# Performance work log

Measured on AMD Instinct MI355X. Metric: run time of the kernel, lower is better.

Reference implementation:

```python
import jax, jax.numpy as jnp
import numpy as np


def setup_inputs() -> dict:
    key = jax.random.key(0)
    ks = jax.random.split(key, 8)
    B, L, D, H = 4, 2048, 4096, 8
    BW = D // H
    std = 1.0 / np.sqrt(BW)
    x = jax.random.normal(ks[0], (B, L, D), dtype=jnp.float32)
    segment_pos = jax.random.randint(ks[1], (B, L), 0, 1024)
    prev_h = jax.random.normal(ks[2], (B, D), dtype=jnp.float32)
    w_in = jax.random.normal(ks[3], (H, BW, BW), dtype=jnp.float32) * std
    b_in = jnp.zeros((H, BW), dtype=jnp.float32)
    w_a = jax.random.normal(ks[4], (H, BW, BW), dtype=jnp.float32) * std
    b_a = jnp.zeros((H, BW), dtype=jnp.float32)
    # a_param init: uniform on ring [0.9, 0.999], softplus-inverse transform
    unif = jax.random.uniform(ks[5], (D,), dtype=jnp.float32)
    min_rad, max_rad = 0.9, 0.999
    a_real = 0.5 * jnp.log(unif * (max_rad**2 - min_rad**2) + min_rad**2 + 1e-8)
    a_param = jnp.log(jnp.exp(-a_real) - 1.0)
    return {"x": x, "segment_pos": segment_pos, "prev_h": prev_h,
            "w_in": w_in, "b_in": b_in, "w_a": w_a, "b_a": b_a,
            "a_param": a_param}


def _block_diag_linear(x, w, b):
    # x: [B,L,D]; w: [H,BW,BW]; b: [H,BW]
    B, L, D = x.shape
    H = w.shape[0]
    xr = x.reshape(B, L, H, D // H)
    y = jnp.einsum('blhi,hij->blhj', xr, w) + b
    return y.reshape(B, L, D)


def reference(x, segment_pos, prev_h, w_in, b_in, w_a, b_a, a_param):
    # reset indicator at document boundaries (segment_pos == 0)
    reset = (segment_pos == 0).astype(x.dtype)          # [B,L]
    gate_x = jax.nn.sigmoid(_block_diag_linear(x, w_in, b_in))
    gate_a = jax.nn.sigmoid(_block_diag_linear(x, w_a, b_a))
    log_a = -8.0 * gate_a * jax.nn.softplus(a_param)    # [B,L,D]
    a = jnp.exp(log_a)
    multiplier = jnp.sqrt(1.0 - jnp.exp(2.0 * log_a) + 1e-6)
    multiplier = reset[..., None] + (1.0 - reset)[..., None] * multiplier
    normalized_x = x * gate_x * multiplier
    # zero the decay at reset positions (hidden state reset)
    a = a * (1.0 - reset)[..., None]
    # linear recurrence y_t = a_t * y_{t-1} + x_t (initial hidden state = 0,
    # matching the torch L>1 path which does not use prev_h)
    def combine(c1, c2):
        a1, b1 = c1
        a2, b2 = c2
        return (a2 * a1, a2 * b1 + b2)
    _, y = jax.lax.associative_scan(combine, (a, normalized_x), axis=1)
    return y
```

## Files before the change

kernel.cpp:

```cpp
#include <hip/hip_runtime.h>
#include <hip/hip_bf16.h>

typedef _Float16 f16;
typedef _Float16 f16x2 __attribute__((ext_vector_type(2)));
typedef _Float16 f16x8 __attribute__((ext_vector_type(8)));
typedef float f32x4 __attribute__((ext_vector_type(4)));

#define B_  4
#define L_  2048
#define D_  4096
#define H_  8
#define BW_ 512
#define M_  (B_*L_)
#define CHUNK 128
#define NCH (L_/CHUNK)
#define LOG2E 1.4426950408889634f

static const size_t OFF_WPK   = 0;
static const size_t OFF_MSP   = 8ull<<20;
static const size_t OFF_XH    = 9ull<<20;
static const size_t OFF_YLAP  = 73ull<<20;
static const size_t OFF_SUMA  = 208ull<<20;
static const size_t OFF_SUMY  = 209ull<<20;

__device__ __forceinline__ void gl16(const void* g, void* l) {
    __builtin_amdgcn_global_load_lds(
        (const __attribute__((address_space(1))) unsigned int*)g,
        (__attribute__((address_space(3))) unsigned int*)l, 16, 0, 0);
}

__global__ __launch_bounds__(256)
void prep_all(const float* __restrict__ w_in, const float* __restrict__ w_a,
              const float* __restrict__ a_param, const float* __restrict__ x,
              f16* __restrict__ wpk, float* __restrict__ msp2,
              f16* __restrict__ xh) {
    const int bid = blockIdx.x;
    const int tid = threadIdx.x;
    if (bid < 1024) {
        const int kt  = bid & 7;
        const int n32 = (bid >> 3) & 15;
        const int h   = bid >> 7;
        if (bid < 16) {
            int d = bid * 256 + tid;
            float v = a_param[d];
            msp2[d] = -8.f * log1pf(expf(v)) * LOG2E;
        }
#pragma unroll
        for (int q = 0; q < 2; ++q) {
            int slot = q * 256 + tid;
            int lane = slot & 63;
            int fidx = slot >> 6;
            int g    = fidx >> 2;
            int fn   = (fidx >> 1) & 1;
            int kk2  = fidx & 1;
            int row = n32 * 32 + fn * 16 + (lane & 15);
            int col = kt * 64 + kk2 * 32 + ((lane >> 4) << 3);
            const float* src = (g ? w_a : w_in) + (size_t)h * BW_ * BW_;
            f16x8 v;
#pragma unroll
            for (int e = 0; e < 8; ++e)
                v[e] = (f16)src[(size_t)(col + e) * BW_ + row];
            size_t o = ((((size_t)(h * 16 + n32) * 8 + kt) * 8) + fidx) * 64 + lane;
            *(f16x8*)(wpk + o * 8) = v;
        }
    } else {
        size_t i = ((size_t)(bid - 1024) * 256 + tid) * 8;
        const size_t stride = (size_t)2048 * 256 * 8;
        for (; i < (size_t)M_ * D_; i += stride) {
            f32x4 v0 = *(const f32x4*)(x + i);
            f32x4 v1 = *(const f32x4*)(x + i + 4);
            f16x8 hv;
            hv[0] = (f16)v0.x; hv[1] = (f16)v0.y; hv[2] = (f16)v0.z; hv[3] = (f16)v0.w;
            hv[4] = (f16)v1.x; hv[5] = (f16)v1.y; hv[6] = (f16)v1.z; hv[7] = (f16)v1.w;
            *(f16x8*)(xh + i) = hv;
        }
    }
}

#define BM 128
#define BN 64
#define BKK 64
#define NT (BW_/BKK)
#define BUFB 16384

#define SMEM_BYTES 52992

__global__ __launch_bounds__(256, 2)
void gemm_gates(const f16*   __restrict__ xh,
                const int*   __restrict__ segpos,
                const f16*   __restrict__ wpk,
                const float* __restrict__ b_in,
                const float* __restrict__ b_a,
                const float* __restrict__ msp2,
                f16x2* __restrict__ ylap,
                float* __restrict__ sumA,
                float* __restrict__ sumY) {
    __shared__ __align__(16) char smem[SMEM_BYTES];
    f16x2* axn  = (f16x2*)(smem + 16384);
    float* segA = (float*)(smem + 50176);
    float* segY = (float*)(smem + 51328);
    float* rst_s= (float*)(smem + 52480);

    const int tid  = threadIdx.x;
    const int m0   = blockIdx.x * BM;
    const int n0   = blockIdx.y * BN;
    const int h    = blockIdx.z;
    const int lane = tid & 63;
    const int wid  = tid >> 6;
    const int wr   = wid >> 1;
    const int wc   = wid & 1;

    f32x4 accX[4][2] = {};
    f32x4 accA[4][2] = {};

    if (tid < BM) rst_s[tid] = (segpos[m0 + tid] == 0) ? 1.f : 0.f;

    const int grow  = lane >> 3;
    const int gcolS = (((lane & 7) ^ grow) << 3);
    const f16* aSrc = xh + (size_t)(m0 + wid * 32 + grow) * D_ + h * BW_ + gcolS;

    const f16* wbase = wpk + ((size_t)(h * 16) + (n0 >> 5) + wc) * 32768;

    const int swz  = (lane & 7) << 3;
    const int kx   = (lane >> 4) << 3;
    const int arow = wr * 64 + (lane & 15);
    const int rowb = wr * 64 + ((lane >> 4) << 2);
    const int txo  = ((n0 >> 6) + 2) & (NT - 1);

    f16x8 bfr[2][8];

#define STAGE_A(T)                                                            \
    {                                                                         \
        const int ktg = ((T) + txo) & (NT - 1);                               \
        f16* Asb = (f16*)(smem + ((T) % 3) * BUFB);                           \
        _Pragma("unroll")                                                     \
        for (int q = 0; q < 4; ++q)                                           \
            gl16(aSrc + ktg * BKK + (size_t)q * 8 * D_,                       \
                 &Asb[(wid * 32 + q * 8) * 64]);                              \
    }
#define LOAD_B(T)                                                             \
    {                                                                         \
        const int ktg = ((T) + txo) & (NT - 1);                               \
        const f16* tp = wbase + (size_t)ktg * 4096;                           \
        _Pragma("unroll")                                                     \
        for (int j = 0; j < 8; ++j)                                           \
            bfr[(T) & 1][j] = *(const f16x8*)(tp + j * 512 + lane * 8);       \
    }

    LOAD_B(0);
    STAGE_A(0);
    STAGE_A(1);

#pragma unroll
    for (int t = 0; t < NT; ++t) {
        if (t == 0)          asm volatile("s_waitcnt vmcnt(4)"  ::: "memory");
        else if (t < NT - 1) asm volatile("s_waitcnt vmcnt(12)" ::: "memory");
        else                 asm volatile("s_waitcnt vmcnt(8)"  ::: "memory");
        __builtin_amdgcn_s_barrier();
        if (t + 1 < NT) LOAD_B(t + 1);
        if (t + 2 < NT) STAGE_A(t + 2);
        __builtin_amdgcn_sched_barrier(0);

        const f16* Asb = (const f16*)(smem + (t % 3) * BUFB);
#pragma unroll
        for (int kk2 = 0; kk2 < 2; ++kk2) {
            const int kcolS = (kk2 * 32 + kx) ^ swz;
            f16x8 af[4];
#pragma unroll
            for (int fm = 0; fm < 4; ++fm)
                af[fm] = *(const f16x8*)&Asb[(arow + fm * 16) * 64 + kcolS];
#pragma unroll
            for (int fn = 0; fn < 2; ++fn) {
                f16x8 bx = bfr[t & 1][fn * 2 + kk2];
                f16x8 ba = bfr[t & 1][4 + fn * 2 + kk2];
#pragma unroll
                for (int fm = 0; fm < 4; ++fm) {
                    accX[fm][fn] = __builtin_amdgcn_mfma_f32_16x16x32_f16(af[fm], bx, accX[fm][fn], 0, 0, 0);
                    accA[fm][fn] = __builtin_amdgcn_mfma_f32_16x16x32_f16(af[fm], ba, accA[fm][fn], 0, 0, 0);
                }
            }
        }
    }
#undef STAGE_A
#undef LOAD_B

    __syncthreads();

    {
#pragma unroll
        for (int fn = 0; fn < 2; ++fn) {
            const int ctile = wc * 32 + fn * 16 + (lane & 15);
            const int d = h * BW_ + n0 + ctile;
            const float bx = b_in[d];
            const float ba = b_a[d];
            const float mspd = msp2[d];
#pragma unroll
            for (int fm = 0; fm < 4; ++fm) {
#pragma unroll
                for (int reg = 0; reg < 4; ++reg) {
                    const int rowt = rowb + fm * 16 + reg;
                    float gxl = accX[fm][fn][reg] + bx;
                    float gal = accA[fm][fn][reg] + ba;
                    float gx = __builtin_amdgcn_rcpf(1.f + __builtin_amdgcn_exp2f(-gxl * LOG2E));
                    float ga = __builtin_amdgcn_rcpf(1.f + __builtin_amdgcn_exp2f(-gal * LOG2E));
                    float a  = __builtin_amdgcn_exp2f(mspd * ga);
                    float a2 = a * a;
                    float mult = __builtin_amdgcn_sqrtf(1.f + 1e-6f - a2);
                    float rv = rst_s[rowt];
                    a *= (1.f - rv);
                    mult = rv + (1.f - rv) * mult;
                    f16x2 p;
                    p[0] = (f16)(1.f - a);
                    p[1] = (f16)(gx * mult);
                    axn[rowt * 66 + ctile] = p;
                }
            }
        }
    }
    __syncthreads();

    const f16* As0 = (const f16*)smem;
    const int col = tid & 63;
    const int seg = tid >> 6;
    {
        float A = 1.f, yv = 0.f;
#pragma unroll 4
        for (int i = 0; i < 32; ++i) {
            const int t = seg * 32 + i;
            f16x2 v = axn[t * 66 + col];
            float a  = 1.f - (float)v[0];
            float xv = (float)As0[t * 64 + (col ^ ((t & 7) << 3))];
            yv = fmaf(a, yv, xv * (float)v[1]);
            A *= a;
        }
        segA[seg * 72 + col] = A;
        segY[seg * 72 + col] = yv;
    }
    __syncthreads();

    {
        float cy = 0.f, pA = 1.f;
        for (int s = 0; s < seg; ++s) {
            float As_ = segA[s * 72 + col];
            cy = fmaf(As_, cy, segY[s * 72 + col]);
            pA *= As_;
        }
        float Arun = 1.f, yv = cy;
        const size_t obase = (size_t)(m0 + seg * 32) * D_ + h * BW_ + n0 + col;
#pragma unroll 4
        for (int i = 0; i < 32; ++i) {
            const int t = seg * 32 + i;
            f16x2 v = axn[t * 66 + col];
            float a  = 1.f - (float)v[0];
            float xv = (float)As0[t * 64 + (col ^ ((t & 7) << 3))];
            yv = fmaf(a, yv, xv * (float)v[1]);
            Arun *= a;
            f16x2 p;
            p[0] = (f16)yv;
            p[1] = (f16)(pA * Arun);
            ylap[obase + (size_t)i * D_] = p;
        }
        if (seg == 3) {
            const int bb = m0 >> 11;
            const int cc = (m0 & 2047) >> 7;
            size_t si = ((size_t)bb * NCH + cc) * D_ + h * BW_ + n0 + col;
            sumA[si] = pA * Arun;
            sumY[si] = yv;
        }
    }
}

__global__ __launch_bounds__(256)
void scan_apply(const float* __restrict__ sumA, const float* __restrict__ sumY,
                const f16x2* __restrict__ ylap, float* __restrict__ y) {
    const int tid = threadIdx.x;
    const int d4  = (blockIdx.x * 256 + tid) * 4;
    const int c   = blockIdx.y >> 2;
    const int tq  = blockIdx.y & 3;
    const int b   = blockIdx.z;
    f32x4 h0 = {0.f, 0.f, 0.f, 0.f};
    for (int cp = 0; cp < c; ++cp) {
        size_t si = (((size_t)(b * NCH + cp)) << 12) + d4;
        f32x4 A = *(const f32x4*)(sumA + si);
        f32x4 Y = *(const f32x4*)(sumY + si);
        h0.x = fmaf(A.x, h0.x, Y.x);
        h0.y = fmaf(A.y, h0.y, Y.y);
        h0.z = fmaf(A.z, h0.z, Y.z);
        h0.w = fmaf(A.w, h0.w, Y.w);
    }
    size_t base = ((size_t)(b * L_ + c * CHUNK + tq * 32)) * D_ + d4;
#pragma unroll 4
    for (int i = 0; i < 32; ++i) {
        size_t o = base + (size_t)i * D_;
        f16x8 p = *(const f16x8*)(ylap + o);
        f32x4 ov;
        ov.x = fmaf(h0.x, (float)p[1], (float)p[0]);
        ov.y = fmaf(h0.y, (float)p[3], (float)p[2]);
        ov.z = fmaf(h0.z, (float)p[5], (float)p[4]);
        ov.w = fmaf(h0.w, (float)p[7], (float)p[6]);
        *(f32x4*)(y + o) = ov;
    }
}

extern "C" void kernel_launch(void* const* d_in, const int* in_sizes, int n_in,
                              void* d_out, int out_size, void* d_ws, size_t ws_size,
                              hipStream_t stream) {
    const float* x       = (const float*)d_in[0];
    const int*   segpos  = (const int*)d_in[1];
    const float* w_in    = (const float*)d_in[3];
    const float* b_in    = (const float*)d_in[4];
    const float* w_a     = (const float*)d_in[5];
    const float* b_a     = (const float*)d_in[6];
    const float* a_param = (const float*)d_in[7];

    float* y  = (float*)d_out;
    char*  ws = (char*)d_ws;
    f16*   wpk   = (f16*)(ws + OFF_WPK);
    float* msp2  = (float*)(ws + OFF_MSP);
    f16*   xh    = (f16*)(ws + OFF_XH);
    f16x2* ylap  = (f16x2*)(ws + OFF_YLAP);
    float* sumA  = (float*)(ws + OFF_SUMA);
    float* sumY  = (float*)(ws + OFF_SUMY);

    prep_all<<<dim3(3072), 256, 0, stream>>>(w_in, w_a, a_param, x, wpk, msp2, xh);
    gemm_gates<<<dim3(M_ / BM, BW_ / BN, H_), 256, 0, stream>>>(
        xh, segpos, wpk, b_in, b_a, msp2, ylap, sumA, sumY);
    scan_apply<<<dim3(D_ / 1024, NCH * 4, B_), 256, 0, stream>>>(sumA, sumY, ylap, y);
}
```

Measured before the change: 214.3 us.

## Switch A staging to double buffering and fold x into gate product

Result: slower. 219.7 us (+2.5%).

```diff
diff --git a/kernel.cpp b/kernel.cpp
--- a/kernel.cpp
+++ b/kernel.cpp
@@ -83,7 +83,7 @@
 #define NT (BW_/BKK)
 #define BUFB 16384
 
-#define SMEM_BYTES 52992
+#define SMEM_BYTES 36608
 
 __global__ __launch_bounds__(256, 2)
 void gemm_gates(const f16*   __restrict__ xh,
@@ -96,10 +96,10 @@
                 float* __restrict__ sumA,
                 float* __restrict__ sumY) {
     __shared__ __align__(16) char smem[SMEM_BYTES];
-    f16x2* axn  = (f16x2*)(smem + 16384);
-    float* segA = (float*)(smem + 50176);
-    float* segY = (float*)(smem + 51328);
-    float* rst_s= (float*)(smem + 52480);
+    f16x2* axn  = (f16x2*)smem;
+    float* segA = (float*)(smem + 33792);
+    float* segY = (float*)(smem + 34944);
+    float* rst_s= (float*)(smem + 36096);
 
     const int tid  = threadIdx.x;
     const int m0   = blockIdx.x * BM;
@@ -125,14 +125,14 @@
     const int kx   = (lane >> 4) << 3;
     const int arow = wr * 64 + (lane & 15);
     const int rowb = wr * 64 + ((lane >> 4) << 2);
-    const int txo  = ((n0 >> 6) + 2) & (NT - 1);
+    const int txo  = ((n0 >> 6) + 1) & (NT - 1);
 
     f16x8 bfr[2][8];
 
 #define STAGE_A(T)                                                            \
     {                                                                         \
         const int ktg = ((T) + txo) & (NT - 1);                               \
-        f16* Asb = (f16*)(smem + ((T) % 3) * BUFB);                           \
+        f16* Asb = (f16*)(smem + ((T) & 1) * BUFB);                           \
         _Pragma("unroll")                                                     \
         for (int q = 0; q < 4; ++q)                                           \
             gl16(aSrc + ktg * BKK + (size_t)q * 8 * D_,                       \
@@ -149,19 +149,15 @@
 
     LOAD_B(0);
     STAGE_A(0);
-    STAGE_A(1);
 
 #pragma unroll
     for (int t = 0; t < NT; ++t) {
-        if (t == 0)          asm volatile("s_waitcnt vmcnt(4)"  ::: "memory");
-        else if (t < NT - 1) asm volatile("s_waitcnt vmcnt(12)" ::: "memory");
-        else                 asm volatile("s_waitcnt vmcnt(8)"  ::: "memory");
+        asm volatile("s_waitcnt vmcnt(0)" ::: "memory");
         __builtin_amdgcn_s_barrier();
-        if (t + 1 < NT) LOAD_B(t + 1);
-        if (t + 2 < NT) STAGE_A(t + 2);
+        if (t + 1 < NT) { LOAD_B(t + 1); STAGE_A(t + 1); }
         __builtin_amdgcn_sched_barrier(0);
 
-        const f16* Asb = (const f16*)(smem + (t % 3) * BUFB);
+        const f16* Asb = (const f16*)(smem + (t & 1) * BUFB);
 #pragma unroll
         for (int kk2 = 0; kk2 < 2; ++kk2) {
             const int kcolS = (kk2 * 32 + kx) ^ swz;
@@ -184,6 +180,19 @@
 #undef STAGE_A
 #undef LOAD_B
 
+    const f16* As1 = (const f16*)(smem + BUFB);
+    f16 xvv[2][4][4];
+#pragma unroll
+    for (int fn = 0; fn < 2; ++fn) {
+        const int ctile = wc * 32 + fn * 16 + (lane & 15);
+#pragma unroll
+        for (int fm = 0; fm < 4; ++fm)
+#pragma unroll
+            for (int reg = 0; reg < 4; ++reg) {
+                const int rowt = rowb + fm * 16 + reg;
+                xvv[fn][fm][reg] = As1[rowt * 64 + (ctile ^ ((rowt & 7) << 3))];
+            }
+    }
     __syncthreads();
 
     {
@@ -209,9 +218,10 @@
                     float rv = rst_s[rowt];
                     a *= (1.f - rv);
                     mult = rv + (1.f - rv) * mult;
+                    float xv = (float)xvv[fn][fm][reg];
                     f16x2 p;
                     p[0] = (f16)(1.f - a);
-                    p[1] = (f16)(gx * mult);
+                    p[1] = (f16)(xv * gx * mult);
                     axn[rowt * 66 + ctile] = p;
                 }
             }
@@ -219,18 +229,15 @@
     }
     __syncthreads();
 
-    const f16* As0 = (const f16*)smem;
     const int col = tid & 63;
     const int seg = tid >> 6;
     {
         float A = 1.f, yv = 0.f;
 #pragma unroll 4
         for (int i = 0; i < 32; ++i) {
-            const int t = seg * 32 + i;
-            f16x2 v = axn[t * 66 + col];
-            float a  = 1.f - (float)v[0];
-            float xv = (float)As0[t * 64 + (col ^ ((t & 7) << 3))];
-            yv = fmaf(a, yv, xv * (float)v[1]);
+            f16x2 v = axn[(seg * 32 + i) * 66 + col];
+            float a = 1.f - (float)v[0];
+            yv = fmaf(a, yv, (float)v[1]);
             A *= a;
         }
         segA[seg * 72 + col] = A;
@@ -249,11 +256,9 @@
         const size_t obase = (size_t)(m0 + seg * 32) * D_ + h * BW_ + n0 + col;
 #pragma unroll 4
         for (int i = 0; i < 32; ++i) {
-            const int t = seg * 32 + i;
-            f16x2 v = axn[t * 66 + col];
-            float a  = 1.f - (float)v[0];
-            float xv = (float)As0[t * 64 + (col ^ ((t & 7) << 3))];
-            yv = fmaf(a, yv, xv * (float)v[1]);
+            f16x2 v = axn[(seg * 32 + i) * 66 + col];
+            float a = 1.f - (float)v[0];
+            yv = fmaf(a, yv, (float)v[1]);
             Arun *= a;
             f16x2 p;
             p[0] = (f16)yv;
```
